# Performance work log

Measured on AMD Instinct MI355X. Metric: run time of the kernel, lower is better.

The kernel has to match this reference:

```python
import jax, jax.numpy as jnp
import numpy as np

H = 300
V = 19495
B = 64
TU = 50
TT = 64


def gru(x, h0, Wih, Whh, bih, bhh, lens=None):
    """PyTorch-equation GRU, batch_first. x:[B,T,H], h0:[B,H].
    If lens is given, emulates pack/pad: outputs are zero past len,
    hidden state stops updating past len (final h = state at last valid step)."""
    Bx, T, _ = x.shape
    xg = jnp.einsum('bth,gh->btg', x, Wih) + bih          # [B,T,3H]
    xg = jnp.transpose(xg, (1, 0, 2))                      # [T,B,3H]
    if lens is None:
        mask = jnp.ones((T, Bx, 1), x.dtype)
    else:
        mask = (jnp.arange(T)[:, None] < lens[None, :]).astype(x.dtype)[..., None]  # [T,B,1]

    def step(h, tm):
        xg_t, m = tm
        hg = h @ Whh.T + bhh
        xr, xz, xn = jnp.split(xg_t, 3, axis=-1)
        hr, hz, hn = jnp.split(hg, 3, axis=-1)
        r = jax.nn.sigmoid(xr + hr)
        z = jax.nn.sigmoid(xz + hz)
        n = jnp.tanh(xn + r * hn)
        h_new = (1.0 - z) * n + z * h
        h = m * h_new + (1.0 - m) * h
        return h, h_new * m

    h_last, outs = jax.lax.scan(step, h0, (xg, mask))
    return jnp.transpose(outs, (1, 0, 2)), h_last


def setup_inputs() -> dict:
    key = jax.random.key(0)
    ks = jax.random.split(key, 24)
    s = 0.05
    p = {}
    p['emb_table'] = jax.random.normal(ks[0], (V, H), jnp.float32) * s
    for i, name in enumerate(['enc', 'sess', 'dec']):
        p[name + '_Wih'] = jax.random.normal(ks[1 + 4 * i], (3 * H, H), jnp.float32) * s
        p[name + '_Whh'] = jax.random.normal(ks[2 + 4 * i], (3 * H, H), jnp.float32) * s
        p[name + '_bih'] = jax.random.normal(ks[3 + 4 * i], (3 * H,), jnp.float32) * s
        p[name + '_bhh'] = jax.random.normal(ks[4 + 4 * i], (3 * H,), jnp.float32) * s
    p['out_W'] = jax.random.normal(ks[13], (V, H), jnp.float32) * s
    p['out_b'] = jax.random.normal(ks[14], (V,), jnp.float32) * s
    p['u1_input'] = jax.random.randint(ks[15], (B, TU), 0, V, jnp.int32)
    p['u1_lens'] = jax.random.randint(ks[16], (B,), 1, TU + 1, jnp.int32)
    p['u2_input'] = jax.random.randint(ks[17], (B, TU), 0, V, jnp.int32)
    p['u2_lens'] = jax.random.randint(ks[18], (B,), 1, TU + 1, jnp.int32)
    p['target_input'] = jax.random.randint(ks[19], (B, TT), 0, V, jnp.int32)
    p['target_input_lens'] = jax.random.randint(ks[20], (B,), 1, TT + 1, jnp.int32)
    return p


def reference(emb_table, enc_Wih, enc_Whh, enc_bih, enc_bhh,
              sess_Wih, sess_Whh, sess_bih, sess_bhh,
              dec_Wih, dec_Whh, dec_bih, dec_bhh,
              out_W, out_b,
              u1_input, u1_lens, u2_input, u2_lens,
              target_input, target_input_lens):
    h0 = jnp.zeros((B, H), jnp.float32)
    # utterance encoders (shared GRU), pack/pad semantics via masking
    _, u1_h = gru(emb_table[u1_input], h0, enc_Wih, enc_Whh, enc_bih, enc_bhh, u1_lens)
    _, u2_h = gru(emb_table[u2_input], h0, enc_Wih, enc_Whh, enc_bih, enc_bhh, u2_lens)
    si = jnp.stack([u1_h, u2_h], axis=1)  # [B,2,H]
    _, sess_h = gru(si, h0, sess_Wih, sess_Whh, sess_bih, sess_bhh)
    # teacher-forced decoder over all target steps
    tgt_emb = emb_table[target_input]      # [B,TT,H]
    dec_outs, _ = gru(tgt_emb, sess_h, dec_Wih, dec_Whh, dec_bih, dec_bhh)
    logits = jnp.einsum('bth,vh->btv', dec_outs, out_W) + out_b  # [B,TT,V]
    return logits
```

## Files before the change

kernel.cpp:

```cpp
#include <hip/hip_runtime.h>
#include <hip/hip_bf16.h>


#define HDIM 300
#define H3   900
#define KP   320
#define NV   19495
#define NVP  19584
#define NB   64
#define TUL  50
#define TTL  64
#define HS   328
#define HFS  301

typedef short short8 __attribute__((ext_vector_type(8)));
typedef float f32x4  __attribute__((ext_vector_type(4)));

__device__ inline unsigned short f32_to_bf16(float f) {
  unsigned int u = __float_as_uint(f);
  u = u + 0x7FFFu + ((u >> 16) & 1u);
  return (unsigned short)(u >> 16);
}

__global__ void convert_pad_kernel(const float* __restrict__ src, short* __restrict__ dst, int rows) {
  int total = rows * HDIM;
  for (int i = blockIdx.x * blockDim.x + threadIdx.x; i < total; i += gridDim.x * blockDim.x) {
    int r = i / HDIM, c = i - r * HDIM;
    dst[(long)r * KP + c] = (short)f32_to_bf16(src[i]);
  }
}

#define GM_PROJ 0
#define GM_XGE  1
#define GM_XGD  2

template <int MODE>
__launch_bounds__(256)
__global__ void mfma_gemm_kernel(const short* __restrict__ A,
                                 const short* __restrict__ B,
                                 const float* __restrict__ bias,
                                 float* __restrict__ C,
                                 const int* __restrict__ idx1,
                                 const int* __restrict__ idx2) {
  __shared__ short Asm[128 * 40];
  __shared__ short Bsm[128 * 40];
  int tid = threadIdx.x;
  int lane = tid & 63, wid = tid >> 6;
  int wm = wid >> 1, wn = wid & 1;
  int m0 = blockIdx.y * 128, n0 = blockIdx.x * 128;

  f32x4 acc[4][4] = {};

  int lrow = tid >> 2, lq = tid & 3;
  long arow[2], brow[2];
#pragma unroll
  for (int h = 0; h < 2; ++h) {
    int m = m0 + lrow + h * 64;
    long rowbase;
    if (MODE == GM_PROJ) {
      rowbase = (long)m * KP;
    } else if (MODE == GM_XGD) {
      rowbase = (long)idx1[m] * KP;
    } else {
      int u = m / 3200;
      int rm = m - u * 3200;
      int b = rm / TUL;
      int t = rm - b * TUL;
      int iv = u ? idx2[b * TUL + t] : idx1[b * TUL + t];
      rowbase = (long)iv * KP;
    }
    arow[h] = rowbase + lq * 8;
    brow[h] = (long)(n0 + lrow + h * 64) * KP + lq * 8;
  }

  for (int k0 = 0; k0 < KP; k0 += 32) {
#pragma unroll
    for (int h = 0; h < 2; ++h) {
      *(short8*)&Asm[(lrow + h * 64) * 40 + lq * 8] = *(const short8*)&A[arow[h] + k0];
      *(short8*)&Bsm[(lrow + h * 64) * 40 + lq * 8] = *(const short8*)&B[brow[h] + k0];
    }
    __syncthreads();
    int rlo = lane & 15, khi = (lane >> 4) * 8;
    short8 af[4], bfv[4];
#pragma unroll
    for (int i = 0; i < 4; ++i) af[i]  = *(const short8*)&Asm[(wm * 64 + i * 16 + rlo) * 40 + khi];
#pragma unroll
    for (int i = 0; i < 4; ++i) bfv[i] = *(const short8*)&Bsm[(wn * 64 + i * 16 + rlo) * 40 + khi];
#pragma unroll
    for (int i = 0; i < 4; ++i)
#pragma unroll
      for (int j = 0; j < 4; ++j)
        acc[i][j] = __builtin_amdgcn_mfma_f32_16x16x32_bf16(af[i], bfv[j], acc[i][j], 0, 0, 0);
    __syncthreads();
  }

  int rhi = (lane >> 4) * 4, cl = lane & 15;
#pragma unroll
  for (int i = 0; i < 4; ++i)
#pragma unroll
    for (int j = 0; j < 4; ++j) {
      int mb = m0 + wm * 64 + i * 16 + rhi;
      int n = n0 + wn * 64 + j * 16 + cl;
#pragma unroll
      for (int r = 0; r < 4; ++r) {
        int m = mb + r;
        float v = acc[i][j][r];
        if (MODE == GM_PROJ) {
          if (n < NV) C[(long)m * NV + n] = v + bias[n];
        } else if (MODE == GM_XGD) {
          if (n < H3) {
            int b = m >> 6, t = m & 63;
            C[(long)t * (H3 * NB) + n * NB + b] = v + bias[n];
          }
        } else {
          if (n < H3) {
            int u = m / 3200;
            int rm = m - u * 3200;
            int b = rm / TUL;
            int t = rm - b * TUL;
            C[(long)t * (H3 * 128) + n * 128 + u * 64 + b] = v + bias[n];
          }
        }
      }
    }
}

__device__ __forceinline__ void run_chunks(const short* __restrict__ Wb,
                                           const short8 (&af)[10],
                                           f32x4 (&acc)[5][3],
                                           int wv, int lane) {
  int jc = lane & 15;
  int kh = (lane >> 4) * 8;
  short8 bb[3][10];
  auto issue = [&](int c, short8 (&buf)[10]) {
    int tw = c / 3, g = c - tw * 3;
    const short* p = Wb + (long)(g * HDIM + (wv + 4 * tw) * 16 + jc) * KP + kh;
#pragma unroll
    for (int kk = 0; kk < 10; ++kk) buf[kk] = *(const short8*)(p + kk * 32);
  };
  issue(0, bb[0]);
  issue(1, bb[1]);
#pragma unroll
  for (int c = 0; c < 15; ++c) {
    if (c + 2 < 15) issue(c + 2, bb[(c + 2) % 3]);
    int tw = c / 3, g = c - tw * 3;
#pragma unroll
    for (int kk = 0; kk < 10; ++kk)
      acc[tw][g] = __builtin_amdgcn_mfma_f32_16x16x32_bf16(af[kk], bb[c % 3][kk], acc[tw][g], 0, 0, 0);
  }
}

template <int MODE>
__device__ __forceinline__ void gru_fused_step(
    int w, int wv, int lane, int t,
    const short* __restrict__ Wb, const float* __restrict__ xg,
    float* __restrict__ hF, short* __restrict__ hbf,
    const float* __restrict__ bhhL, const float* __restrict__ xgS,
    const int* __restrict__ lensL, short* __restrict__ abf) {
  int jc = lane & 15, kh = (lane >> 4) * 8, mh = lane >> 4;
  short8 af[10];
#pragma unroll
  for (int kk = 0; kk < 10; ++kk)
    af[kk] = *(const short8*)&hbf[jc * HS + kk * 32 + kh];
  __syncthreads();
  f32x4 acc[5][3];
#pragma unroll
  for (int a = 0; a < 5; ++a)
#pragma unroll
    for (int g = 0; g < 3; ++g) acc[a][g] = (f32x4){0.f, 0.f, 0.f, 0.f};
  run_chunks(Wb, af, acc, wv, lane);
#pragma unroll
  for (int tw = 0; tw < 5; ++tw) {
    int jm = (wv + 4 * tw) * 16 + jc;
    bool jok = jm < HDIM;
    int j = jok ? jm : 0;
    float br = bhhL[j], bz = bhhL[HDIM + j], bn = bhhL[2 * HDIM + j];
#pragma unroll
    for (int r = 0; r < 4; ++r) {
      int m = mh * 4 + r;
      float XR, XZ, XN;
      if (MODE == 0) {
        int col = (m < 8) ? (8 * w + m) : (64 + 8 * w + (m - 8));
        const float* b = xg + ((long)t * H3 + j) * 128 + col;
        XR = b[0]; XZ = b[HDIM * 128]; XN = b[2 * HDIM * 128];
      } else if (MODE == 1) {
        int col = 8 * w + (m & 7);
        const float* b = xg + ((long)t * H3 + j) * NB + col;
        XR = b[0]; XZ = b[HDIM * NB]; XN = b[2 * HDIM * NB];
      } else {
        XR = xgS[(0 * KP + j) * 17 + m];
        XZ = xgS[(1 * KP + j) * 17 + m];
        XN = xgS[(2 * KP + j) * 17 + m];
      }
      float HRv = acc[tw][0][r] + br;
      float HZv = acc[tw][1][r] + bz;
      float HNv = acc[tw][2][r] + bn;
      float rg = 1.f / (1.f + __expf(-(XR + HRv)));
      float zg = 1.f / (1.f + __expf(-(XZ + HZv)));
      float ng = tanhf(XN + rg * HNv);
      float hp = hF[m * HFS + j];
      float hnew = (1.f - zg) * ng + zg * hp;
      if (MODE == 0 && t >= lensL[m]) hnew = hp;
      bool mok = (MODE == 0) || (m < 8);
      if (jok && mok) {
        hF[m * HFS + jm] = hnew;
        short hb = (short)f32_to_bf16(hnew);
        hbf[m * HS + jm] = hb;
        if (MODE == 1) abf[((long)(8 * w + m) * TTL + t) * KP + jm] = hb;
      }
    }
  }
  __syncthreads();
}

__launch_bounds__(256, 1)
__global__ void fused_recurrence_kernel(
    const short* __restrict__ WhhE, const short* __restrict__ WhhSs,
    const short* __restrict__ WihSs, const short* __restrict__ WhhD,
    const float* __restrict__ bhhE_g, const float* __restrict__ bhhS_g,
    const float* __restrict__ bihS_g, const float* __restrict__ bhhD_g,
    const float* __restrict__ xgE, const float* __restrict__ xgD,
    const int* __restrict__ u1l, const int* __restrict__ u2l,
    short* __restrict__ abf) {
  __shared__ float hF1[16 * HFS];
  __shared__ short hb1[16 * HS];
  __shared__ float hF2[16 * HFS];
  __shared__ short hb2[16 * HS];
  __shared__ float xgS[3 * KP * 17];
  __shared__ float bhhL[H3];
  __shared__ int lensL[16];
  int tid = threadIdx.x, lane = tid & 63, wv = tid >> 6, w = blockIdx.x;

  for (int i = tid; i < 16 * HFS; i += 256) { hF1[i] = 0.f; hF2[i] = 0.f; }
  for (int i = tid; i < 16 * HS; i += 256) { hb1[i] = 0; hb2[i] = 0; }
  if (tid < 8) lensL[tid] = u1l[8 * w + tid];
  else if (tid < 16) lensL[tid] = u2l[8 * w + tid - 8];
  for (int i = tid; i < H3; i += 256) bhhL[i] = bhhE_g[i];
  __syncthreads();

  for (int t = 0; t < TUL; ++t)
    gru_fused_step<0>(w, wv, lane, t, WhhE, xgE, hF1, hb1, bhhL, nullptr, lensL, nullptr);

  for (int i = tid; i < H3; i += 256) bhhL[i] = bhhS_g[i];
  __syncthreads();
  for (int t = 0; t < 2; ++t) {
    {
      int jc = lane & 15, kh = (lane >> 4) * 8, mh = lane >> 4;
      int xrow = 8 * t + (jc & 7);
      short8 af[10];
#pragma unroll
      for (int kk = 0; kk < 10; ++kk)
        af[kk] = *(const short8*)&hb1[xrow * HS + kk * 32 + kh];
      f32x4 acc[5][3];
#pragma unroll
      for (int a = 0; a < 5; ++a)
#pragma unroll
        for (int g = 0; g < 3; ++g) acc[a][g] = (f32x4){0.f, 0.f, 0.f, 0.f};
      run_chunks(WihSs, af, acc, wv, lane);
#pragma unroll
      for (int tw = 0; tw < 5; ++tw) {
        int jm = (wv + 4 * tw) * 16 + jc;
        if (jm < HDIM) {
#pragma unroll
          for (int g = 0; g < 3; ++g) {
            float bi = bihS_g[g * HDIM + jm];
#pragma unroll
            for (int r = 0; r < 4; ++r)
              xgS[(g * KP + jm) * 17 + (mh * 4 + r)] = acc[tw][g][r] + bi;
          }
        }
      }
      __syncthreads();
    }
    gru_fused_step<2>(w, wv, lane, t, WhhSs, nullptr, hF2, hb2, bhhL, xgS, nullptr, nullptr);
  }

  for (int i = tid; i < H3; i += 256) bhhL[i] = bhhD_g[i];
  __syncthreads();
  for (int t = 0; t < TTL; ++t)
    gru_fused_step<1>(w, wv, lane, t, WhhD, xgD, hF2, hb2, bhhL, nullptr, nullptr, abf);
}

extern "C" void kernel_launch(void* const* d_in, const int* in_sizes, int n_in,
                              void* d_out, int out_size, void* d_ws, size_t ws_size,
                              hipStream_t stream) {
  const float* emb      = (const float*)d_in[0];
  const float* enc_Wih  = (const float*)d_in[1];
  const float* enc_Whh  = (const float*)d_in[2];
  const float* enc_bih  = (const float*)d_in[3];
  const float* enc_bhh  = (const float*)d_in[4];
  const float* sess_Wih = (const float*)d_in[5];
  const float* sess_Whh = (const float*)d_in[6];
  const float* sess_bih = (const float*)d_in[7];
  const float* sess_bhh = (const float*)d_in[8];
  const float* dec_Wih  = (const float*)d_in[9];
  const float* dec_Whh  = (const float*)d_in[10];
  const float* dec_bih  = (const float*)d_in[11];
  const float* dec_bhh  = (const float*)d_in[12];
  const float* out_W    = (const float*)d_in[13];
  const float* out_b    = (const float*)d_in[14];
  const int* u1_in      = (const int*)d_in[15];
  const int* u1_lens    = (const int*)d_in[16];
  const int* u2_in      = (const int*)d_in[17];
  const int* u2_lens    = (const int*)d_in[18];
  const int* tgt_in     = (const int*)d_in[19];
  float* out = (float*)d_out;

  char* w = (char*)d_ws;
  auto alloc = [&](size_t bytes) -> char* {
    char* p = w;
    w += (bytes + 255) & ~(size_t)255;
    return p;
  };
  short* emb_bf  = (short*)alloc((size_t)NV  * KP * 2);
  short* wie_bf  = (short*)alloc((size_t)1024 * KP * 2);
  short* wid_bf  = (short*)alloc((size_t)1024 * KP * 2);
  short* wout_bf = (short*)alloc((size_t)NVP * KP * 2);
  short* a_bf    = (short*)alloc((size_t)4096 * KP * 2);
  short* whhE_bf = (short*)alloc((size_t)960 * KP * 2);
  short* whhS_bf = (short*)alloc((size_t)960 * KP * 2);
  short* wihS_bf = (short*)alloc((size_t)960 * KP * 2);
  short* whhD_bf = (short*)alloc((size_t)960 * KP * 2);
  char* bf_end = w;
  float* xg_enc = (float*)alloc((size_t)TUL * H3 * 128 * 4);
  float* xg_dec = (float*)alloc((size_t)TTL * H3 * NB * 4);

  hipMemsetAsync(emb_bf, 0, (size_t)(bf_end - (char*)emb_bf), stream);

  convert_pad_kernel<<<1024, 256, 0, stream>>>(emb, emb_bf, NV);
  convert_pad_kernel<<<64, 256, 0, stream>>>(enc_Wih, wie_bf, H3);
  convert_pad_kernel<<<64, 256, 0, stream>>>(dec_Wih, wid_bf, H3);
  convert_pad_kernel<<<1024, 256, 0, stream>>>(out_W, wout_bf, NV);
  convert_pad_kernel<<<64, 256, 0, stream>>>(enc_Whh, whhE_bf, H3);
  convert_pad_kernel<<<64, 256, 0, stream>>>(sess_Whh, whhS_bf, H3);
  convert_pad_kernel<<<64, 256, 0, stream>>>(sess_Wih, wihS_bf, H3);
  convert_pad_kernel<<<64, 256, 0, stream>>>(dec_Whh, whhD_bf, H3);

  {
    dim3 g(8, 50);
    mfma_gemm_kernel<GM_XGE><<<g, 256, 0, stream>>>(emb_bf, wie_bf, enc_bih, xg_enc, u1_in, u2_in);
  }
  {
    dim3 g(8, 32);
    mfma_gemm_kernel<GM_XGD><<<g, 256, 0, stream>>>(emb_bf, wid_bf, dec_bih, xg_dec, tgt_in, nullptr);
  }

  fused_recurrence_kernel<<<8, 256, 0, stream>>>(
      whhE_bf, whhS_bf, wihS_bf, whhD_bf,
      enc_bhh, sess_bhh, sess_bih, dec_bhh,
      xg_enc, xg_dec, u1_lens, u2_lens, a_bf);

  {
    dim3 g(153, 32);
    mfma_gemm_kernel<GM_PROJ><<<g, 256, 0, stream>>>(a_bf, wout_bf, out_b, out, nullptr, nullptr);
  }
}
```

Baseline: 3.029 ms.

## Split GRU recurrence across eight waves with double-buffered hidden state

The fused recurrence kernel grows from 4 to 8 waves per block. Each wave now owns 2 or 3 column tiles instead of 5, and weights stream in half-K chunks. The bf16 hidden state is double-buffered so each timestep needs one barrier instead of two. The xg gate inputs are loaded into registers before the MFMA loop, and all three bias vectors are staged once at kernel start. The goal is to cut per-step latency in the serial recurrence, at the cost of more register pressure and uneven work across waves.

```diff
diff --git a/kernel.cpp b/kernel.cpp
--- a/kernel.cpp
+++ b/kernel.cpp
@@ -125,79 +125,85 @@
     }
 }
 
-__device__ __forceinline__ void run_chunks(const short* __restrict__ Wb,
-                                           const short8 (&af)[10],
-                                           f32x4 (&acc)[5][3],
-                                           int wv, int lane) {
+template <int NT>
+__device__ __forceinline__ void run_chunks8(const short* __restrict__ Wb,
+                                            const short8 (&af)[10],
+                                            f32x4 (&acc)[NT][3],
+                                            const int (&tiles)[3], int lane) {
   int jc = lane & 15;
   int kh = (lane >> 4) * 8;
-  short8 bb[3][10];
-  auto issue = [&](int c, short8 (&buf)[10]) {
-    int tw = c / 3, g = c - tw * 3;
-    const short* p = Wb + (long)(g * HDIM + (wv + 4 * tw) * 16 + jc) * KP + kh;
-#pragma unroll
-    for (int kk = 0; kk < 10; ++kk) buf[kk] = *(const short8*)(p + kk * 32);
+  short8 bb[3][5];
+  auto issue = [&](int hc, short8 (&buf)[5]) {
+    int c = hc >> 1, hh = hc & 1;
+    int ti = c / 3, g = c - ti * 3;
+    const short* p = Wb + (long)(g * HDIM + tiles[ti] * 16 + jc) * KP + hh * 160 + kh;
+#pragma unroll
+    for (int kk = 0; kk < 5; ++kk) buf[kk] = *(const short8*)(p + kk * 32);
   };
   issue(0, bb[0]);
   issue(1, bb[1]);
 #pragma unroll
-  for (int c = 0; c < 15; ++c) {
-    if (c + 2 < 15) issue(c + 2, bb[(c + 2) % 3]);
-    int tw = c / 3, g = c - tw * 3;
-#pragma unroll
-    for (int kk = 0; kk < 10; ++kk)
-      acc[tw][g] = __builtin_amdgcn_mfma_f32_16x16x32_bf16(af[kk], bb[c % 3][kk], acc[tw][g], 0, 0, 0);
-  }
-}
-
-template <int MODE>
-__device__ __forceinline__ void gru_fused_step(
-    int w, int wv, int lane, int t,
+  for (int hc = 0; hc < NT * 6; ++hc) {
+    if (hc + 2 < NT * 6) issue(hc + 2, bb[(hc + 2) % 3]);
+    int c = hc >> 1, hh = hc & 1, ti = c / 3, g = c - ti * 3;
+#pragma unroll
+    for (int kk = 0; kk < 5; ++kk)
+      acc[ti][g] = __builtin_amdgcn_mfma_f32_16x16x32_bf16(af[hh * 5 + kk], bb[hc % 3][kk], acc[ti][g], 0, 0, 0);
+  }
+}
+
+template <int NT, int MODE>
+__device__ __forceinline__ void gru_step8(
+    int w, int lane, const int (&tiles)[3], int t,
     const short* __restrict__ Wb, const float* __restrict__ xg,
-    float* __restrict__ hF, short* __restrict__ hbf,
-    const float* __restrict__ bhhL, const float* __restrict__ xgS,
-    const int* __restrict__ lensL, short* __restrict__ abf) {
+    float (&xgv)[3][3][4],
+    float* __restrict__ hF, const short* __restrict__ hbf_r, short* __restrict__ hbf_w,
+    const float* __restrict__ bhhL, const int* __restrict__ lensL,
+    short* __restrict__ abf) {
   int jc = lane & 15, kh = (lane >> 4) * 8, mh = lane >> 4;
+  if (MODE != 2) {
+#pragma unroll
+    for (int ti = 0; ti < NT; ++ti) {
+      int jm = tiles[ti] * 16 + jc;
+      int j = (jm < HDIM) ? jm : 0;
+#pragma unroll
+      for (int g = 0; g < 3; ++g) {
+        const float* p = xg + ((long)t * H3 + g * HDIM + j) * (MODE == 0 ? 128 : NB);
+#pragma unroll
+        for (int r = 0; r < 4; ++r) {
+          int m = mh * 4 + r;
+          int col = (MODE == 0) ? ((m < 8) ? (8 * w + m) : (64 + 8 * w + (m - 8)))
+                                : (8 * w + (m & 7));
+          xgv[ti][g][r] = p[col];
+        }
+      }
+    }
+  }
   short8 af[10];
 #pragma unroll
   for (int kk = 0; kk < 10; ++kk)
-    af[kk] = *(const short8*)&hbf[jc * HS + kk * 32 + kh];
-  __syncthreads();
-  f32x4 acc[5][3];
-#pragma unroll
-  for (int a = 0; a < 5; ++a)
+    af[kk] = *(const short8*)&hbf_r[jc * HS + kk * 32 + kh];
+  f32x4 acc[NT][3];
+#pragma unroll
+  for (int a = 0; a < NT; ++a)
 #pragma unroll
     for (int g = 0; g < 3; ++g) acc[a][g] = (f32x4){0.f, 0.f, 0.f, 0.f};
-  run_chunks(Wb, af, acc, wv, lane);
-#pragma unroll
-  for (int tw = 0; tw < 5; ++tw) {
-    int jm = (wv + 4 * tw) * 16 + jc;
+  run_chunks8<NT>(Wb, af, acc, tiles, lane);
+#pragma unroll
+  for (int ti = 0; ti < NT; ++ti) {
+    int jm = tiles[ti] * 16 + jc;
     bool jok = jm < HDIM;
     int j = jok ? jm : 0;
     float br = bhhL[j], bz = bhhL[HDIM + j], bn = bhhL[2 * HDIM + j];
 #pragma unroll
     for (int r = 0; r < 4; ++r) {
       int m = mh * 4 + r;
-      float XR, XZ, XN;
-      if (MODE == 0) {
-        int col = (m < 8) ? (8 * w + m) : (64 + 8 * w + (m - 8));
-        const float* b = xg + ((long)t * H3 + j) * 128 + col;
-        XR = b[0]; XZ = b[HDIM * 128]; XN = b[2 * HDIM * 128];
-      } else if (MODE == 1) {
-        int col = 8 * w + (m & 7);
-        const float* b = xg + ((long)t * H3 + j) * NB + col;
-        XR = b[0]; XZ = b[HDIM * NB]; XN = b[2 * HDIM * NB];
-      } else {
-        XR = xgS[(0 * KP + j) * 17 + m];
-        XZ = xgS[(1 * KP + j) * 17 + m];
-        XN = xgS[(2 * KP + j) * 17 + m];
-      }
-      float HRv = acc[tw][0][r] + br;
-      float HZv = acc[tw][1][r] + bz;
-      float HNv = acc[tw][2][r] + bn;
-      float rg = 1.f / (1.f + __expf(-(XR + HRv)));
-      float zg = 1.f / (1.f + __expf(-(XZ + HZv)));
-      float ng = tanhf(XN + rg * HNv);
+      float HRv = acc[ti][0][r] + br;
+      float HZv = acc[ti][1][r] + bz;
+      float HNv = acc[ti][2][r] + bn;
+      float rg = 1.f / (1.f + __expf(-(xgv[ti][0][r] + HRv)));
+      float zg = 1.f / (1.f + __expf(-(xgv[ti][1][r] + HZv)));
+      float ng = tanhf(xgv[ti][2][r] + rg * HNv);
       float hp = hF[m * HFS + j];
       float hnew = (1.f - zg) * ng + zg * hp;
       if (MODE == 0 && t >= lensL[m]) hnew = hp;
@@ -205,15 +211,44 @@
       if (jok && mok) {
         hF[m * HFS + jm] = hnew;
         short hb = (short)f32_to_bf16(hnew);
-        hbf[m * HS + jm] = hb;
+        hbf_w[m * HS + jm] = hb;
         if (MODE == 1) abf[((long)(8 * w + m) * TTL + t) * KP + jm] = hb;
       }
     }
   }
-  __syncthreads();
-}
-
-__launch_bounds__(256, 1)
+}
+
+template <int NT>
+__device__ __forceinline__ void sess_xg8(
+    int lane, const int (&tiles)[3], int t,
+    const short* __restrict__ WihSs, const short* __restrict__ hb1f,
+    const float* __restrict__ bihS_g, float (&xgv)[3][3][4]) {
+  int jc = lane & 15, kh = (lane >> 4) * 8;
+  int xrow = 8 * t + (jc & 7);
+  short8 af[10];
+#pragma unroll
+  for (int kk = 0; kk < 10; ++kk)
+    af[kk] = *(const short8*)&hb1f[xrow * HS + kk * 32 + kh];
+  f32x4 acc[NT][3];
+#pragma unroll
+  for (int a = 0; a < NT; ++a)
+#pragma unroll
+    for (int g = 0; g < 3; ++g) acc[a][g] = (f32x4){0.f, 0.f, 0.f, 0.f};
+  run_chunks8<NT>(WihSs, af, acc, tiles, lane);
+#pragma unroll
+  for (int ti = 0; ti < NT; ++ti) {
+    int jm = tiles[ti] * 16 + jc;
+    int j = (jm < HDIM) ? jm : 0;
+#pragma unroll
+    for (int g = 0; g < 3; ++g) {
+      float bi = bihS_g[g * HDIM + j];
+#pragma unroll
+      for (int r = 0; r < 4; ++r) xgv[ti][g][r] = acc[ti][g][r] + bi;
+    }
+  }
+}
+
+__launch_bounds__(512, 2)
 __global__ void fused_recurrence_kernel(
     const short* __restrict__ WhhE, const short* __restrict__ WhhSs,
     const short* __restrict__ WihSs, const short* __restrict__ WhhD,
@@ -223,62 +258,48 @@
     const int* __restrict__ u1l, const int* __restrict__ u2l,
     short* __restrict__ abf) {
   __shared__ float hF1[16 * HFS];
-  __shared__ short hb1[16 * HS];
+  __shared__ short hb1[2][16 * HS];
   __shared__ float hF2[16 * HFS];
-  __shared__ short hb2[16 * HS];
-  __shared__ float xgS[3 * KP * 17];
-  __shared__ float bhhL[H3];
+  __shared__ short hb2[2][16 * HS];
+  __shared__ float bhhA[3][H3];
   __shared__ int lensL[16];
   int tid = threadIdx.x, lane = tid & 63, wv = tid >> 6, w = blockIdx.x;
 
-  for (int i = tid; i < 16 * HFS; i += 256) { hF1[i] = 0.f; hF2[i] = 0.f; }
-  for (int i = tid; i < 16 * HS; i += 256) { hb1[i] = 0; hb2[i] = 0; }
+  for (int i = tid; i < 16 * HFS; i += 512) { hF1[i] = 0.f; hF2[i] = 0.f; }
+  for (int i = tid; i < 16 * HS; i += 512) { hb1[0][i] = 0; hb1[1][i] = 0; hb2[0][i] = 0; hb2[1][i] = 0; }
   if (tid < 8) lensL[tid] = u1l[8 * w + tid];
   else if (tid < 16) lensL[tid] = u2l[8 * w + tid - 8];
-  for (int i = tid; i < H3; i += 256) bhhL[i] = bhhE_g[i];
+  for (int i = tid; i < H3; i += 512) {
+    bhhA[0][i] = bhhE_g[i]; bhhA[1][i] = bhhS_g[i]; bhhA[2][i] = bhhD_g[i];
+  }
   __syncthreads();
 
-  for (int t = 0; t < TUL; ++t)
-    gru_fused_step<0>(w, wv, lane, t, WhhE, xgE, hF1, hb1, bhhL, nullptr, lensL, nullptr);
-
-  for (int i = tid; i < H3; i += 256) bhhL[i] = bhhS_g[i];
-  __syncthreads();
+  int tiles[3] = {wv, wv + 8, 16 + (wv & 3)};
+  bool n3 = wv < 4;
+  float xgv[3][3][4];
+
+  for (int t = 0; t < TUL; ++t) {
+    if (n3) gru_step8<3, 0>(w, lane, tiles, t, WhhE, xgE, xgv, hF1, hb1[t & 1], hb1[(t + 1) & 1], bhhA[0], lensL, nullptr);
+    else    gru_step8<2, 0>(w, lane, tiles, t, WhhE, xgE, xgv, hF1, hb1[t & 1], hb1[(t + 1) & 1], bhhA[0], lensL, nullptr);
+    __syncthreads();
+  }
+
   for (int t = 0; t < 2; ++t) {
-    {
-      int jc = lane & 15, kh = (lane >> 4) * 8, mh = lane >> 4;
-      int xrow = 8 * t + (jc & 7);
-      short8 af[10];
-#pragma unroll
-      for (int kk = 0; kk < 10; ++kk)
-        af[kk] = *(const short8*)&hb1[xrow * HS + kk * 32 + kh];
-      f32x4 acc[5][3];
-#pragma unroll
-      for (int a = 0; a < 5; ++a)
-#pragma unroll
-        for (int g = 0; g < 3; ++g) acc[a][g] = (f32x4){0.f, 0.f, 0.f, 0.f};
-      run_chunks(WihSs, af, acc, wv, lane);
-#pragma unroll
-      for (int tw = 0; tw < 5; ++tw) {
-        int jm = (wv + 4 * tw) * 16 + jc;
-        if (jm < HDIM) {
-#pragma unroll
-          for (int g = 0; g < 3; ++g) {
-            float bi = bihS_g[g * HDIM + jm];
-#pragma unroll
-            for (int r = 0; r < 4; ++r)
-              xgS[(g * KP + jm) * 17 + (mh * 4 + r)] = acc[tw][g][r] + bi;
-          }
-        }
-      }
-      __syncthreads();
-    }
-    gru_fused_step<2>(w, wv, lane, t, WhhSs, nullptr, hF2, hb2, bhhL, xgS, nullptr, nullptr);
-  }
-
-  for (int i = tid; i < H3; i += 256) bhhL[i] = bhhD_g[i];
-  __syncthreads();
-  for (int t = 0; t < TTL; ++t)
-    gru_fused_step<1>(w, wv, lane, t, WhhD, xgD, hF2, hb2, bhhL, nullptr, nullptr, abf);
+    if (n3) {
+      sess_xg8<3>(lane, tiles, t, WihSs, hb1[0], bihS_g, xgv);
+      gru_step8<3, 2>(w, lane, tiles, t, WhhSs, nullptr, xgv, hF2, hb2[t & 1], hb2[(t + 1) & 1], bhhA[1], nullptr, nullptr);
+    } else {
+      sess_xg8<2>(lane, tiles, t, WihSs, hb1[0], bihS_g, xgv);
+      gru_step8<2, 2>(w, lane, tiles, t, WhhSs, nullptr, xgv, hF2, hb2[t & 1], hb2[(t + 1) & 1], bhhA[1], nullptr, nullptr);
+    }
+    __syncthreads();
+  }
+
+  for (int t = 0; t < TTL; ++t) {
+    if (n3) gru_step8<3, 1>(w, lane, tiles, t, WhhD, xgD, xgv, hF2, hb2[t & 1], hb2[(t + 1) & 1], bhhA[2], nullptr, abf);
+    else    gru_step8<2, 1>(w, lane, tiles, t, WhhD, xgD, xgv, hF2, hb2[t & 1], hb2[(t + 1) & 1], bhhA[2], nullptr, abf);
+    __syncthreads();
+  }
 }
 
 extern "C" void kernel_launch(void* const* d_in, const int* in_sizes, int n_in,
@@ -345,7 +366,7 @@
     mfma_gemm_kernel<GM_XGD><<<g, 256, 0, stream>>>(emb_bf, wid_bf, dec_bih, xg_dec, tgt_in, nullptr);
   }
 
-  fused_recurrence_kernel<<<8, 256, 0, stream>>>(
+  fused_recurrence_kernel<<<8, 512, 0, stream>>>(
       whhE_bf, whhS_bf, wihS_bf, whhD_bf,
       enc_bhh, sess_bhh, sess_bih, dec_bhh,
       xg_enc, xg_dec, u1_lens, u2_lens, a_bf);
```

New measurement: 2.913 ms. 3.8% less time.
